# Optimization experiments

Hardware: AMD Instinct MI355X
Metric: run time of the kernel (lower is better)

## Reference

```python
import jax, jax.numpy as jnp
import numpy as np

B, N, D, H = 4, 1024, 1024, 16
HD = D // H
SCALE = HD ** -0.5


def setup_inputs() -> dict:
    key = jax.random.key(0)
    ks = jax.random.split(key, 12)
    s = 0.02
    return {
        "q": jax.random.normal(ks[0], (B, N, D), jnp.float32),
        "k": jax.random.normal(ks[1], (B, N, D), jnp.float32),
        "v": jax.random.normal(ks[2], (B, N, D), jnp.float32),
        "rel_pos_emb": jax.random.normal(ks[3], (N, N, HD), jnp.float32) * s,
        "Wq": jax.random.normal(ks[4], (D, D), jnp.float32) * s,
        "bq": jnp.zeros((D,), jnp.float32),
        "Wk": jax.random.normal(ks[5], (D, D), jnp.float32) * s,
        "bk": jnp.zeros((D,), jnp.float32),
        "Wv": jax.random.normal(ks[6], (D, D), jnp.float32) * s,
        "bv": jnp.zeros((D,), jnp.float32),
        "Wo": jax.random.normal(ks[7], (D, D), jnp.float32) * s,
        "bo": jnp.zeros((D,), jnp.float32),
    }


def reference(q, k, v, rel_pos_emb, Wq, bq, Wk, bk, Wv, bv, Wo, bo):
    # Linear projections (torch Linear: x @ W.T + b)
    qp = q @ Wq.T + bq
    kp = k @ Wk.T + bk
    vp = v @ Wv.T + bv
    # [b, n, (h d)] -> [b, h, n, d]
    split = lambda t: t.reshape(t.shape[0], t.shape[1], H, HD).transpose(0, 2, 1, 3)
    qh = split(qp) * SCALE
    kh = split(kp)
    vh = split(vp)
    # content scores + relative-position scores (rel_pos_emb is [q,k,d];
    # the b,h repeat in the original is a pure broadcast, folded into einsum)
    attn = jnp.einsum('bhqd,bhkd->bhqk', qh, kh)
    attn = attn + jnp.einsum('bhqd,qkd->bhqk', qh, rel_pos_emb)
    attn = jax.nn.softmax(attn, axis=-1)  # dropout p=0.0 (eval): identity
    out = jnp.einsum('bhqk,bhkd->bhqd', attn, vh)
    out = out.transpose(0, 2, 1, 3).reshape(B, N, D)  # [b,h,n,d] -> [b,n,(h d)]
    return out @ Wo.T + bo
```

## Files before the change

### kernel.cpp

```cpp
#include <hip/hip_runtime.h>
#include <hip/hip_bf16.h>

#define NB 4
#define SEQ 1024
#define DM 1024
#define NH 16
#define HD 64
#define QSCALE 0.125f
#define NTOK (NB*SEQ)

using f32x4  = __attribute__((ext_vector_type(4))) float;
using bf16x8 = __attribute__((ext_vector_type(8))) short;
using s16x4  = __attribute__((ext_vector_type(4))) short;

__device__ __forceinline__ short f2bf(float x){
  __hip_bfloat16 h = __float2bfloat16(x);
  return *reinterpret_cast<short*>(&h);
}
__device__ __forceinline__ float bf2f(short x){
  __hip_bfloat16 h; *reinterpret_cast<short*>(&h) = x;
  return __bfloat162float(h);
}
__device__ __forceinline__ unsigned char f2fp8(float x){
  int d = __builtin_amdgcn_cvt_pk_fp8_f32(x, x, 0, false);
  return (unsigned char)(d & 0xff);
}
__device__ __forceinline__ float fp82f(unsigned char x){
  return __builtin_amdgcn_cvt_f32_fp8((int)x, 0);
}

__device__ __forceinline__ void gld16(const void* g, void* l){
  __builtin_amdgcn_global_load_lds(
      (const __attribute__((address_space(1))) unsigned int*)g,
      (__attribute__((address_space(3))) unsigned int*)l, 16, 0, 0);
}

__global__ void cvt_all(const float* __restrict__ a0, const float* __restrict__ a1,
                        const float* __restrict__ a2, const float* __restrict__ a3,
                        const float* __restrict__ a4, const float* __restrict__ a5,
                        const float* __restrict__ a6,
                        short* o0, short* o1, short* o2, short* o3,
                        short* o4, short* o5, short* o6, int big4, int small4){
  int i = blockIdx.x * blockDim.x + threadIdx.x;
  int y = blockIdx.y;
  int n4 = (y < 3) ? big4 : small4;
  if (i >= n4) return;
  const float* in; short* out;
  if      (y == 0){ in = a0; out = o0; }
  else if (y == 1){ in = a1; out = o1; }
  else if (y == 2){ in = a2; out = o2; }
  else if (y == 3){ in = a3; out = o3; }
  else if (y == 4){ in = a4; out = o4; }
  else if (y == 5){ in = a5; out = o5; }
  else            { in = a6; out = o6; }
  float4 v = reinterpret_cast<const float4*>(in)[i];
  s16x4 o;
  o[0] = f2bf(v.x); o[1] = f2bf(v.y); o[2] = f2bf(v.z); o[3] = f2bf(v.w);
  reinterpret_cast<s16x4*>(out)[i] = o;
}

__global__ __launch_bounds__(256) void proj_gemm(
    const short* __restrict__ qb, const short* __restrict__ kb, const short* __restrict__ vb,
    const short* __restrict__ wqb, const short* __restrict__ wkb, const short* __restrict__ wvb,
    const float* __restrict__ bq, const float* __restrict__ bk, const float* __restrict__ bv,
    short* __restrict__ qhb, short* __restrict__ khb, short* __restrict__ vTb)
{
  __shared__ short As[128*32];
  __shared__ short Bs[128*32];
  const int t = threadIdx.x, w = t >> 6, l = t & 63, lr = l & 15, lg = l >> 4;
  const int wr = w >> 1, wc = w & 1;
  const int which = blockIdx.y >> 3;
  const short *A, *Bt;
  int m0, n0;
  if (which == 2){ A = wvb; Bt = vb; m0 = (blockIdx.y & 7)*128; n0 = blockIdx.x*128; }
  else if (which == 1){ A = kb; Bt = wkb; m0 = blockIdx.x*128; n0 = (blockIdx.y & 7)*128; }
  else { A = qb; Bt = wqb; m0 = blockIdx.x*128; n0 = (blockIdx.y & 7)*128; }
  f32x4 acc[4][4] = {};
  for (int k0 = 0; k0 < DM; k0 += 32){
    __syncthreads();
    #pragma unroll
    for (int i = 0; i < 2; ++i){
      int c = i*256 + t, row = c >> 2, sl = c & 3;
      gld16(A  + (size_t)(m0 + row)*DM + k0 + sl*8, &As[c*8]);
      gld16(Bt + (size_t)(n0 + row)*DM + k0 + sl*8, &Bs[c*8]);
    }
    __syncthreads();
    bf16x8 af[4], bfr[4];
    #pragma unroll
    for (int m = 0; m < 4; ++m)
      af[m] = *reinterpret_cast<const bf16x8*>(&As[(wr*64 + m*16 + lr)*32 + lg*8]);
    #pragma unroll
    for (int n = 0; n < 4; ++n)
      bfr[n] = *reinterpret_cast<const bf16x8*>(&Bs[(wc*64 + n*16 + lr)*32 + lg*8]);
    #pragma unroll
    for (int m = 0; m < 4; ++m)
      #pragma unroll
      for (int n = 0; n < 4; ++n)
        acc[m][n] = __builtin_amdgcn_mfma_f32_16x16x32_bf16(af[m], bfr[n], acc[m][n], 0, 0, 0);
  }
  #pragma unroll
  for (int m = 0; m < 4; ++m){
    int row = m0 + wr*64 + m*16 + lg*4;
    #pragma unroll
    for (int n = 0; n < 4; ++n){
      int col = n0 + wc*64 + n*16 + lr;
      #pragma unroll
      for (int e = 0; e < 4; ++e){
        if (which == 0)
          qhb[(size_t)(row + e)*DM + col] = f2bf((acc[m][n][e] + bq[col]) * QSCALE);
        else if (which == 1)
          khb[(size_t)(row + e)*DM + col] = f2bf(acc[m][n][e] + bk[col]);
        else
          vTb[(size_t)(row + e)*NTOK + col] = f2bf(acc[m][n][e] + bv[row + e]);
      }
    }
  }
}

__global__ __launch_bounds__(256) void out_gemm(const short* __restrict__ A,
    const short* __restrict__ Bt, const float* __restrict__ bias, float* __restrict__ out)
{
  __shared__ short As[128*32];
  __shared__ short Bs[128*32];
  const int t = threadIdx.x, w = t >> 6, l = t & 63, lr = l & 15, lg = l >> 4;
  const int wr = w >> 1, wc = w & 1;
  const int m0 = blockIdx.x*128, n0 = blockIdx.y*128;
  f32x4 acc[4][4] = {};
  for (int k0 = 0; k0 < DM; k0 += 32){
    __syncthreads();
    #pragma unroll
    for (int i = 0; i < 2; ++i){
      int c = i*256 + t, row = c >> 2, sl = c & 3;
      gld16(A  + (size_t)(m0 + row)*DM + k0 + sl*8, &As[c*8]);
      gld16(Bt + (size_t)(n0 + row)*DM + k0 + sl*8, &Bs[c*8]);
    }
    __syncthreads();
    bf16x8 af[4], bfr[4];
    #pragma unroll
    for (int m = 0; m < 4; ++m)
      af[m] = *reinterpret_cast<const bf16x8*>(&As[(wr*64 + m*16 + lr)*32 + lg*8]);
    #pragma unroll
    for (int n = 0; n < 4; ++n)
      bfr[n] = *reinterpret_cast<const bf16x8*>(&Bs[(wc*64 + n*16 + lr)*32 + lg*8]);
    #pragma unroll
    for (int m = 0; m < 4; ++m)
      #pragma unroll
      for (int n = 0; n < 4; ++n)
        acc[m][n] = __builtin_amdgcn_mfma_f32_16x16x32_bf16(af[m], bfr[n], acc[m][n], 0, 0, 0);
  }
  #pragma unroll
  for (int m = 0; m < 4; ++m){
    int row = m0 + wr*64 + m*16 + lg*4;
    #pragma unroll
    for (int n = 0; n < 4; ++n){
      int col = n0 + wc*64 + n*16 + lr;
      float bb = bias[col];
      #pragma unroll
      for (int e = 0; e < 4; ++e)
        out[(size_t)(row + e)*DM + col] = acc[m][n][e] + bb;
    }
  }
}

__global__ __launch_bounds__(256) void relscore2(const short* __restrict__ qh,
    const float* __restrict__ rel, unsigned char* __restrict__ Rs)
{
  __shared__ short At[64*72];
  __shared__ short Bs[64*72];
  const int t = threadIdx.x, w = t >> 6, l = t & 63, lr = l & 15, lg = l >> 4;
  const int q = blockIdx.x;
  #pragma unroll
  for (int i = 0; i < 2; ++i){
    int c = t + i*256;
    int row = c >> 3, off = (c & 7) * 8;
    int b = row >> 4, h = row & 15;
    uint4 v = *reinterpret_cast<const uint4*>(qh + ((size_t)(b*SEQ + q)*NH + h)*HD + off);
    *reinterpret_cast<uint4*>(&At[row*72 + off]) = v;
  }
  __syncthreads();
  bf16x8 af[2];
  af[0] = *reinterpret_cast<const bf16x8*>(&At[(w*16 + lr)*72 + lg*8]);
  af[1] = *reinterpret_cast<const bf16x8*>(&At[(w*16 + lr)*72 + 32 + lg*8]);
  for (int k0 = 0; k0 < SEQ; k0 += 64){
    __syncthreads();
    #pragma unroll
    for (int i = 0; i < 4; ++i){
      int c = t + i*256;
      int row = c >> 4, off = (c & 15) * 4;
      float4 v = *reinterpret_cast<const float4*>(rel + ((size_t)q*SEQ + k0 + row)*HD + off);
      s16x4 o;
      o[0] = f2bf(v.x); o[1] = f2bf(v.y); o[2] = f2bf(v.z); o[3] = f2bf(v.w);
      *reinterpret_cast<s16x4*>(&Bs[row*72 + off]) = o;
    }
    __syncthreads();
    f32x4 acc[4] = {};
    #pragma unroll
    for (int s = 0; s < 2; ++s){
      #pragma unroll
      for (int tt = 0; tt < 4; ++tt){
        bf16x8 bf = *reinterpret_cast<const bf16x8*>(&Bs[(tt*16 + lr)*72 + s*32 + lg*8]);
        acc[tt] = __builtin_amdgcn_mfma_f32_16x16x32_bf16(af[s], bf, acc[tt], 0, 0, 0);
      }
    }
    #pragma unroll
    for (int tt = 0; tt < 4; ++tt){
      #pragma unroll
      for (int e = 0; e < 4; ++e){
        int bh = w*16 + lg*4 + e;
        Rs[((size_t)q*64 + bh)*SEQ + k0 + tt*16 + lr] = f2fp8(acc[tt][e]);
      }
    }
  }
}

__global__ __launch_bounds__(256) void flash2(const short* __restrict__ qh,
    const short* __restrict__ kh, const short* __restrict__ vT,
    const unsigned char* __restrict__ Rs, short* __restrict__ ao)
{
  __shared__ short Kt[128*64];
  __shared__ short Vt[64*128];
  __shared__ short Pt[64*136];
  const int t = threadIdx.x, w = t >> 6, l = t & 63, lr = l & 15, lg = l >> 4;
  const int bh = blockIdx.x, b = bh >> 4, h = bh & 15;
  const int q0 = blockIdx.y * 64;
  bf16x8 qf[2];
  {
    const short* qbase = qh + ((size_t)(b*SEQ + (q0 + w*16 + lr))*NH + h)*HD;
    qf[0] = *reinterpret_cast<const bf16x8*>(qbase + lg*8);
    qf[1] = *reinterpret_cast<const bf16x8*>(qbase + 32 + lg*8);
  }
  f32x4 oacc[4] = {};
  float lrow[4] = {0.f, 0.f, 0.f, 0.f};
  for (int kt = 0; kt < SEQ/128; ++kt){
    const int kbase = kt * 128;
    __syncthreads();
    #pragma unroll
    for (int i = 0; i < 4; ++i){
      int c = i*256 + t, row = c >> 3, sl = c & 7;
      gld16(kh + (size_t)(b*SEQ + kbase + row)*DM + h*HD + 8*(sl ^ (row & 7)), &Kt[c*8]);
    }
    #pragma unroll
    for (int i = 0; i < 4; ++i){
      int c = i*256 + t, row = c >> 4, sl = c & 15;
      gld16(vT + (size_t)(h*HD + row)*NTOK + b*SEQ + kbase + 8*(sl ^ (row & 15)), &Vt[c*8]);
    }
    f32x4 sa[8];
    #pragma unroll
    for (int tt = 0; tt < 8; ++tt)
      #pragma unroll
      for (int e = 0; e < 4; ++e){
        int row = q0 + w*16 + lg*4 + e;
        sa[tt][e] = fp82f(Rs[((size_t)row*64 + bh)*SEQ + kbase + tt*16 + lr]);
      }
    __syncthreads();
    #pragma unroll
    for (int s = 0; s < 2; ++s)
      #pragma unroll
      for (int tt = 0; tt < 8; ++tt){
        int krow = tt*16 + lr;
        bf16x8 kf = *reinterpret_cast<const bf16x8*>(&Kt[krow*64 + 8*((s*4 + lg) ^ (krow & 7))]);
        sa[tt] = __builtin_amdgcn_mfma_f32_16x16x32_bf16(qf[s], kf, sa[tt], 0, 0, 0);
      }
    float rs_[4] = {0.f, 0.f, 0.f, 0.f};
    #pragma unroll
    for (int tt = 0; tt < 8; ++tt)
      #pragma unroll
      for (int e = 0; e < 4; ++e){
        float p = __expf(sa[tt][e]);
        rs_[e] += p;
        Pt[(w*16 + lg*4 + e)*136 + tt*16 + lr] = f2bf(p);
      }
    #pragma unroll
    for (int e = 0; e < 4; ++e){
      #pragma unroll
      for (int mm = 1; mm < 16; mm <<= 1)
        rs_[e] += __shfl_xor(rs_[e], mm, 16);
      lrow[e] += rs_[e];
    }
    #pragma unroll
    for (int ks = 0; ks < 4; ++ks){
      bf16x8 pa = *reinterpret_cast<const bf16x8*>(&Pt[(w*16 + lr)*136 + ks*32 + lg*8]);
      #pragma unroll
      for (int tt = 0; tt < 4; ++tt){
        int vrow = tt*16 + lr;
        bf16x8 vf = *reinterpret_cast<const bf16x8*>(&Vt[vrow*128 + 8*((ks*4 + lg) ^ (vrow & 15))]);
        oacc[tt] = __builtin_amdgcn_mfma_f32_16x16x32_bf16(pa, vf, oacc[tt], 0, 0, 0);
      }
    }
  }
  #pragma unroll
  for (int tt = 0; tt < 4; ++tt){
    #pragma unroll
    for (int e = 0; e < 4; ++e){
      int q = q0 + w*16 + lg*4 + e;
      int hd = tt*16 + lr;
      ao[((size_t)(b*SEQ + q))*DM + h*HD + hd] = f2bf(oacc[tt][e] / lrow[e]);
    }
  }
}

extern "C" void kernel_launch(void* const* d_in, const int* in_sizes, int n_in,
                              void* d_out, int out_size, void* d_ws, size_t ws_size,
                              hipStream_t stream)
{
  const float* q   = (const float*)d_in[0];
  const float* k   = (const float*)d_in[1];
  const float* v   = (const float*)d_in[2];
  const float* rel = (const float*)d_in[3];
  const float* Wq  = (const float*)d_in[4];
  const float* bq  = (const float*)d_in[5];
  const float* Wk  = (const float*)d_in[6];
  const float* bk  = (const float*)d_in[7];
  const float* Wv  = (const float*)d_in[8];
  const float* bv  = (const float*)d_in[9];
  const float* Wo  = (const float*)d_in[10];
  const float* bo  = (const float*)d_in[11];
  float* out = (float*)d_out;

  char* ws = (char*)d_ws;
  short* qb  = (short*)(ws);
  short* kb  = (short*)(ws + 8388608);
  short* vb  = (short*)(ws + 16777216);
  short* qhb = (short*)(ws + 25165824);
  short* khb = (short*)(ws + 33554432);
  short* vTb = (short*)(ws + 41943040);
  short* aob = (short*)(ws + 50331648);
  short* wqb = (short*)(ws + 58720256);
  short* wkb = (short*)(ws + 60817408);
  short* wvb = (short*)(ws + 62914560);
  short* wob = (short*)(ws + 65011712);
  unsigned char* Rs = (unsigned char*)(ws + 67108864);

  dim3 blk(256);
  {
    int big4 = NTOK*DM/4, small4 = DM*DM/4;
    cvt_all<<<dim3(big4/256, 7), blk, 0, stream>>>(q, k, v, Wq, Wk, Wv, Wo,
        qb, kb, vb, wqb, wkb, wvb, wob, big4, small4);
  }
  proj_gemm<<<dim3(NTOK/128, 24), blk, 0, stream>>>(qb, kb, vb, wqb, wkb, wvb,
      bq, bk, bv, qhb, khb, vTb);
  relscore2<<<dim3(SEQ), blk, 0, stream>>>(qhb, rel, Rs);
  flash2<<<dim3(NB*NH, SEQ/64), blk, 0, stream>>>(qhb, khb, vTb, Rs, aob);
  out_gemm<<<dim3(NTOK/128, DM/128), blk, 0, stream>>>(aob, wob, bo, out);
}
```

Baseline: 235.6 us.

## Widen GEMM K-tile with XOR swizzle and transpose flash score MFMA for vector loads

```diff
diff --git a/kernel.cpp b/kernel.cpp
--- a/kernel.cpp
+++ b/kernel.cpp
@@ -24,9 +24,6 @@
 __device__ __forceinline__ unsigned char f2fp8(float x){
   int d = __builtin_amdgcn_cvt_pk_fp8_f32(x, x, 0, false);
   return (unsigned char)(d & 0xff);
-}
-__device__ __forceinline__ float fp82f(unsigned char x){
-  return __builtin_amdgcn_cvt_f32_fp8((int)x, 0);
 }
 
 __device__ __forceinline__ void gld16(const void* g, void* l){
@@ -65,8 +62,8 @@
     const float* __restrict__ bq, const float* __restrict__ bk, const float* __restrict__ bv,
     short* __restrict__ qhb, short* __restrict__ khb, short* __restrict__ vTb)
 {
-  __shared__ short As[128*32];
-  __shared__ short Bs[128*32];
+  __shared__ short As[128*64];
+  __shared__ short Bs[128*64];
   const int t = threadIdx.x, w = t >> 6, l = t & 63, lr = l & 15, lg = l >> 4;
   const int wr = w >> 1, wc = w & 1;
   const int which = blockIdx.y >> 3;
@@ -76,27 +73,31 @@
   else if (which == 1){ A = kb; Bt = wkb; m0 = blockIdx.x*128; n0 = (blockIdx.y & 7)*128; }
   else { A = qb; Bt = wqb; m0 = blockIdx.x*128; n0 = (blockIdx.y & 7)*128; }
   f32x4 acc[4][4] = {};
-  for (int k0 = 0; k0 < DM; k0 += 32){
-    __syncthreads();
-    #pragma unroll
-    for (int i = 0; i < 2; ++i){
-      int c = i*256 + t, row = c >> 2, sl = c & 3;
-      gld16(A  + (size_t)(m0 + row)*DM + k0 + sl*8, &As[c*8]);
-      gld16(Bt + (size_t)(n0 + row)*DM + k0 + sl*8, &Bs[c*8]);
-    }
-    __syncthreads();
-    bf16x8 af[4], bfr[4];
-    #pragma unroll
-    for (int m = 0; m < 4; ++m)
-      af[m] = *reinterpret_cast<const bf16x8*>(&As[(wr*64 + m*16 + lr)*32 + lg*8]);
-    #pragma unroll
-    for (int n = 0; n < 4; ++n)
-      bfr[n] = *reinterpret_cast<const bf16x8*>(&Bs[(wc*64 + n*16 + lr)*32 + lg*8]);
-    #pragma unroll
-    for (int m = 0; m < 4; ++m)
+  for (int k0 = 0; k0 < DM; k0 += 64){
+    __syncthreads();
+    #pragma unroll
+    for (int i = 0; i < 4; ++i){
+      int c = i*256 + t, row = c >> 3, sl = c & 7;
+      int sc = 8 * (sl ^ (row & 7));
+      gld16(A  + (size_t)(m0 + row)*DM + k0 + sc, &As[c*8]);
+      gld16(Bt + (size_t)(n0 + row)*DM + k0 + sc, &Bs[c*8]);
+    }
+    __syncthreads();
+    #pragma unroll
+    for (int s = 0; s < 2; ++s){
+      bf16x8 af[4], bfr[4];
+      #pragma unroll
+      for (int m = 0; m < 4; ++m)
+        af[m] = *reinterpret_cast<const bf16x8*>(&As[(wr*64 + m*16 + lr)*64 + 8*((s*4 + lg) ^ (lr & 7))]);
       #pragma unroll
       for (int n = 0; n < 4; ++n)
-        acc[m][n] = __builtin_amdgcn_mfma_f32_16x16x32_bf16(af[m], bfr[n], acc[m][n], 0, 0, 0);
+        bfr[n] = *reinterpret_cast<const bf16x8*>(&Bs[(wc*64 + n*16 + lr)*64 + 8*((s*4 + lg) ^ (lr & 7))]);
+      #pragma unroll
+      for (int m = 0; m < 4; ++m)
+        #pragma unroll
+        for (int n = 0; n < 4; ++n)
+          acc[m][n] = __builtin_amdgcn_mfma_f32_16x16x32_bf16(af[m], bfr[n], acc[m][n], 0, 0, 0);
+    }
   }
   #pragma unroll
   for (int m = 0; m < 4; ++m){
@@ -120,33 +121,37 @@
 __global__ __launch_bounds__(256) void out_gemm(const short* __restrict__ A,
     const short* __restrict__ Bt, const float* __restrict__ bias, float* __restrict__ out)
 {
-  __shared__ short As[128*32];
-  __shared__ short Bs[128*32];
+  __shared__ short As[128*64];
+  __shared__ short Bs[128*64];
   const int t = threadIdx.x, w = t >> 6, l = t & 63, lr = l & 15, lg = l >> 4;
   const int wr = w >> 1, wc = w & 1;
   const int m0 = blockIdx.x*128, n0 = blockIdx.y*128;
   f32x4 acc[4][4] = {};
-  for (int k0 = 0; k0 < DM; k0 += 32){
-    __syncthreads();
-    #pragma unroll
-    for (int i = 0; i < 2; ++i){
-      int c = i*256 + t, row = c >> 2, sl = c & 3;
-      gld16(A  + (size_t)(m0 + row)*DM + k0 + sl*8, &As[c*8]);
-      gld16(Bt + (size_t)(n0 + row)*DM + k0 + sl*8, &Bs[c*8]);
-    }
-    __syncthreads();
-    bf16x8 af[4], bfr[4];
-    #pragma unroll
-    for (int m = 0; m < 4; ++m)
-      af[m] = *reinterpret_cast<const bf16x8*>(&As[(wr*64 + m*16 + lr)*32 + lg*8]);
-    #pragma unroll
-    for (int n = 0; n < 4; ++n)
-      bfr[n] = *reinterpret_cast<const bf16x8*>(&Bs[(wc*64 + n*16 + lr)*32 + lg*8]);
-    #pragma unroll
-    for (int m = 0; m < 4; ++m)
+  for (int k0 = 0; k0 < DM; k0 += 64){
+    __syncthreads();
+    #pragma unroll
+    for (int i = 0; i < 4; ++i){
+      int c = i*256 + t, row = c >> 3, sl = c & 7;
+      int sc = 8 * (sl ^ (row & 7));
+      gld16(A  + (size_t)(m0 + row)*DM + k0 + sc, &As[c*8]);
+      gld16(Bt + (size_t)(n0 + row)*DM + k0 + sc, &Bs[c*8]);
+    }
+    __syncthreads();
+    #pragma unroll
+    for (int s = 0; s < 2; ++s){
+      bf16x8 af[4], bfr[4];
+      #pragma unroll
+      for (int m = 0; m < 4; ++m)
+        af[m] = *reinterpret_cast<const bf16x8*>(&As[(wr*64 + m*16 + lr)*64 + 8*((s*4 + lg) ^ (lr & 7))]);
       #pragma unroll
       for (int n = 0; n < 4; ++n)
-        acc[m][n] = __builtin_amdgcn_mfma_f32_16x16x32_bf16(af[m], bfr[n], acc[m][n], 0, 0, 0);
+        bfr[n] = *reinterpret_cast<const bf16x8*>(&Bs[(wc*64 + n*16 + lr)*64 + 8*((s*4 + lg) ^ (lr & 7))]);
+      #pragma unroll
+      for (int m = 0; m < 4; ++m)
+        #pragma unroll
+        for (int n = 0; n < 4; ++n)
+          acc[m][n] = __builtin_amdgcn_mfma_f32_16x16x32_bf16(af[m], bfr[n], acc[m][n], 0, 0, 0);
+    }
   }
   #pragma unroll
   for (int m = 0; m < 4; ++m){
@@ -213,7 +218,7 @@
   }
 }
 
-__global__ __launch_bounds__(256) void flash2(const short* __restrict__ qh,
+__global__ __launch_bounds__(256) void flash3(const short* __restrict__ qh,
     const short* __restrict__ kh, const short* __restrict__ vT,
     const unsigned char* __restrict__ Rs, short* __restrict__ ao)
 {
@@ -229,8 +234,10 @@
     qf[0] = *reinterpret_cast<const bf16x8*>(qbase + lg*8);
     qf[1] = *reinterpret_cast<const bf16x8*>(qbase + 32 + lg*8);
   }
+  const unsigned char* rsrow = Rs + ((size_t)(q0 + w*16 + lr)*64 + bh)*SEQ;
+  short* ptrow = &Pt[(w*16 + lr)*136];
   f32x4 oacc[4] = {};
-  float lrow[4] = {0.f, 0.f, 0.f, 0.f};
+  float lsum = 0.f;
   for (int kt = 0; kt < SEQ/128; ++kt){
     const int kbase = kt * 128;
     __syncthreads();
@@ -246,44 +253,43 @@
     }
     f32x4 sa[8];
     #pragma unroll
-    for (int tt = 0; tt < 8; ++tt)
-      #pragma unroll
-      for (int e = 0; e < 4; ++e){
-        int row = q0 + w*16 + lg*4 + e;
-        sa[tt][e] = fp82f(Rs[((size_t)row*64 + bh)*SEQ + kbase + tt*16 + lr]);
-      }
+    for (int tt = 0; tt < 8; ++tt){
+      int rv = *reinterpret_cast<const int*>(rsrow + kbase + tt*16 + lg*4);
+      sa[tt][0] = __builtin_amdgcn_cvt_f32_fp8(rv, 0);
+      sa[tt][1] = __builtin_amdgcn_cvt_f32_fp8(rv, 1);
+      sa[tt][2] = __builtin_amdgcn_cvt_f32_fp8(rv, 2);
+      sa[tt][3] = __builtin_amdgcn_cvt_f32_fp8(rv, 3);
+    }
     __syncthreads();
     #pragma unroll
     for (int s = 0; s < 2; ++s)
       #pragma unroll
       for (int tt = 0; tt < 8; ++tt){
-        int krow = tt*16 + lr;
-        bf16x8 kf = *reinterpret_cast<const bf16x8*>(&Kt[krow*64 + 8*((s*4 + lg) ^ (krow & 7))]);
-        sa[tt] = __builtin_amdgcn_mfma_f32_16x16x32_bf16(qf[s], kf, sa[tt], 0, 0, 0);
-      }
-    float rs_[4] = {0.f, 0.f, 0.f, 0.f};
-    #pragma unroll
-    for (int tt = 0; tt < 8; ++tt)
-      #pragma unroll
-      for (int e = 0; e < 4; ++e){
-        float p = __expf(sa[tt][e]);
-        rs_[e] += p;
-        Pt[(w*16 + lg*4 + e)*136 + tt*16 + lr] = f2bf(p);
-      }
-    #pragma unroll
-    for (int e = 0; e < 4; ++e){
-      #pragma unroll
-      for (int mm = 1; mm < 16; mm <<= 1)
-        rs_[e] += __shfl_xor(rs_[e], mm, 16);
-      lrow[e] += rs_[e];
-    }
+        bf16x8 kf = *reinterpret_cast<const bf16x8*>(&Kt[(tt*16 + lr)*64 + 8*((s*4 + lg) ^ (lr & 7))]);
+        sa[tt] = __builtin_amdgcn_mfma_f32_16x16x32_bf16(kf, qf[s], sa[tt], 0, 0, 0);
+      }
+    float rs = 0.f;
+    #pragma unroll
+    for (int tt = 0; tt < 8; ++tt){
+      #pragma unroll
+      for (int i = 0; i < 2; ++i){
+        float p0 = __expf(sa[tt][2*i]);
+        float p1 = __expf(sa[tt][2*i + 1]);
+        rs += p0 + p1;
+        unsigned int dw = (unsigned int)(unsigned short)f2bf(p0) |
+                          ((unsigned int)(unsigned short)f2bf(p1) << 16);
+        *reinterpret_cast<unsigned int*>(ptrow + tt*16 + lg*4 + 2*i) = dw;
+      }
+    }
+    rs += __shfl_xor(rs, 16);
+    rs += __shfl_xor(rs, 32);
+    lsum += rs;
     #pragma unroll
     for (int ks = 0; ks < 4; ++ks){
-      bf16x8 pa = *reinterpret_cast<const bf16x8*>(&Pt[(w*16 + lr)*136 + ks*32 + lg*8]);
+      bf16x8 pa = *reinterpret_cast<const bf16x8*>(ptrow + ks*32 + lg*8);
       #pragma unroll
       for (int tt = 0; tt < 4; ++tt){
-        int vrow = tt*16 + lr;
-        bf16x8 vf = *reinterpret_cast<const bf16x8*>(&Vt[vrow*128 + 8*((ks*4 + lg) ^ (vrow & 15))]);
+        bf16x8 vf = *reinterpret_cast<const bf16x8*>(&Vt[(tt*16 + lr)*128 + 8*((ks*4 + lg) ^ (lr & 15))]);
         oacc[tt] = __builtin_amdgcn_mfma_f32_16x16x32_bf16(pa, vf, oacc[tt], 0, 0, 0);
       }
     }
@@ -292,9 +298,10 @@
   for (int tt = 0; tt < 4; ++tt){
     #pragma unroll
     for (int e = 0; e < 4; ++e){
+      float ls = __shfl(lsum, 4*lg + e, 16);
       int q = q0 + w*16 + lg*4 + e;
       int hd = tt*16 + lr;
-      ao[((size_t)(b*SEQ + q))*DM + h*HD + hd] = f2bf(oacc[tt][e] / lrow[e]);
+      ao[((size_t)(b*SEQ + q))*DM + h*HD + hd] = f2bf(oacc[tt][e] / ls);
     }
   }
 }
@@ -340,6 +347,6 @@
   proj_gemm<<<dim3(NTOK/128, 24), blk, 0, stream>>>(qb, kb, vb, wqb, wkb, wvb,
       bq, bk, bv, qhb, khb, vTb);
   relscore2<<<dim3(SEQ), blk, 0, stream>>>(qhb, rel, Rs);
-  flash2<<<dim3(NB*NH, SEQ/64), blk, 0, stream>>>(qhb, khb, vTb, Rs, aob);
+  flash3<<<dim3(NB*NH, SEQ/64), blk, 0, stream>>>(qhb, khb, vTb, Rs, aob);
   out_gemm<<<dim3(NTOK/128, DM/128), blk, 0, stream>>>(aob, wob, bo, out);
 }
```

New measurement: 253.2 us. 7.5% more time.
